# Optimization experiments

Hardware: AMD Instinct MI355X
Metric: run time of the kernel (lower is better)

The kernel has to match this reference:

```python
import jax, jax.numpy as jnp
import numpy as np

N_NODES = 50000
N_EDGES = 800000
N_POS = 200000
N_NEG = 200000
D_IN = 128
D_OUT = 128
NEG_SLOPE = 0.2  # DGL GATConv default leaky_relu slope


def setup_inputs() -> dict:
    key = jax.random.key(0)
    ks = jax.random.split(key, 12)
    inp = {
        "x": jax.random.normal(ks[0], (N_NODES, D_IN), dtype=jnp.float32),
        "W": jax.random.normal(ks[1], (D_IN, D_OUT), dtype=jnp.float32) / np.sqrt(D_IN),
        "attn_l": jax.random.normal(ks[2], (D_OUT,), dtype=jnp.float32) / np.sqrt(D_OUT),
        "attn_r": jax.random.normal(ks[3], (D_OUT,), dtype=jnp.float32) / np.sqrt(D_OUT),
        "bias": jnp.zeros((D_OUT,), dtype=jnp.float32),
        "src": jax.random.randint(ks[4], (N_EDGES,), 0, N_NODES, dtype=jnp.int32),
        "dst": jax.random.randint(ks[5], (N_EDGES,), 0, N_NODES, dtype=jnp.int32),
        "pos_src": jax.random.randint(ks[6], (N_POS,), 0, N_NODES, dtype=jnp.int32),
        "pos_dst": jax.random.randint(ks[7], (N_POS,), 0, N_NODES, dtype=jnp.int32),
        "neg_src": jax.random.randint(ks[8], (N_NEG,), 0, N_NODES, dtype=jnp.int32),
        "neg_dst": jax.random.randint(ks[9], (N_NEG,), 0, N_NODES, dtype=jnp.int32),
    }
    return inp


def _gat_conv(x, W, attn_l, attn_r, bias, src, dst):
    # DGL GATConv, num_heads=1, feat_drop=0, activation=relu
    feat = x @ W                               # [N, D_OUT]
    el = feat @ attn_l                         # [N]
    er = feat @ attn_r                         # [N]
    e = jax.nn.leaky_relu(el[src] + er[dst], NEG_SLOPE)  # [E]
    # edge softmax grouped by destination node
    m = jax.ops.segment_max(e, dst, num_segments=N_NODES)   # [N]
    ee = jnp.exp(e - m[dst])
    s = jax.ops.segment_sum(ee, dst, num_segments=N_NODES)  # [N]
    a = ee / s[dst]                            # [E]
    # weighted message aggregation
    h = jax.ops.segment_sum(a[:, None] * feat[src], dst, num_segments=N_NODES)
    return jax.nn.relu(h + bias)               # [N, D_OUT]


def reference(x, W, attn_l, attn_r, bias, src, dst, pos_src, pos_dst, neg_src, neg_dst):
    h = _gat_conv(x, W, attn_l, attn_r, bias, src, dst)
    # ScorePredictor: u_dot_v on each scoring graph -> [E, 1]
    pos_score = jnp.sum(h[pos_src] * h[pos_dst], axis=-1, keepdims=True)
    neg_score = jnp.sum(h[neg_src] * h[neg_dst], axis=-1, keepdims=True)
    return (pos_score, neg_score)
```

## Files before the change

kernel.cpp:

```cpp
#include <hip/hip_runtime.h>
#include <hip/hip_bf16.h>
#include <cstdint>
#include <cstddef>

#define N_NODES 50000
#define N_EDGES 800000
#define N_POS   200000
#define N_NEG   200000
#define DIM     128
#define NEG_SLOPE 0.2f

#define BUCK_SHIFT 5
#define BUCK_NODES 32
#define NBUCK 1563
#define SLABCAP 768
#define BIN_CHUNK 2048
#define NB_BIN 391
#define N_EDGE4 200000

typedef _Float16 half8 __attribute__((ext_vector_type(8)));
typedef float    floatx4 __attribute__((ext_vector_type(4)));

__global__ __launch_bounds__(256) void gemm_feat(
    const float* __restrict__ x, const float* __restrict__ W,
    const float* __restrict__ attn_l, const float* __restrict__ attn_r,
    half8* __restrict__ feat16, float* __restrict__ el, float* __restrict__ er,
    int n)
{
  __shared__ _Float16 xt[64 * 128];
  __shared__ _Float16 wt[128 * 128];
  const int tid = threadIdx.x;
  const int row0 = blockIdx.x * 64;
  const int lane = tid & 63;
  const int wv = tid >> 6;
  const int ql = lane & 15;
  const int quad = lane >> 4;

  {
    const int k = tid >> 1;
    const int n0 = (tid & 1) * 64;
#pragma unroll 4
    for (int j = 0; j < 64; j += 4) {
      const float4 v = *(const float4*)&W[(size_t)k * DIM + n0 + j];
      const float vv[4] = {v.x, v.y, v.z, v.w};
#pragma unroll
      for (int u = 0; u < 4; ++u) {
        const int nn = n0 + j + u;
        wt[nn * 128 + ((((k >> 3) ^ (nn & 15)) << 3) | (k & 7))] = (_Float16)vv[u];
      }
    }
  }
  {
    const int r = tid >> 2;
    const int grow = row0 + r;
    const int c0 = (tid & 3) * 32;
#pragma unroll
    for (int cc = 0; cc < 32; cc += 8) {
      const int c = c0 + cc;
      float4 v0 = make_float4(0.f, 0.f, 0.f, 0.f);
      float4 v1 = make_float4(0.f, 0.f, 0.f, 0.f);
      if (grow < n) {
        const float* sp = &x[(size_t)grow * DIM + c];
        v0 = *(const float4*)(sp);
        v1 = *(const float4*)(sp + 4);
      }
      half8 h;
      h[0] = (_Float16)v0.x; h[1] = (_Float16)v0.y;
      h[2] = (_Float16)v0.z; h[3] = (_Float16)v0.w;
      h[4] = (_Float16)v1.x; h[5] = (_Float16)v1.y;
      h[6] = (_Float16)v1.z; h[7] = (_Float16)v1.w;
      const int chunk = c >> 3;
      *(half8*)&xt[r * 128 + ((chunk ^ (r & 15)) << 3)] = h;
    }
  }
  __syncthreads();

  floatx4 acc[8];
#pragma unroll
  for (int t = 0; t < 8; ++t) acc[t] = (floatx4){0.f, 0.f, 0.f, 0.f};

  const int arow = wv * 16 + ql;
  half8 af[4];
#pragma unroll
  for (int s = 0; s < 4; ++s) {
    const int chunk = s * 4 + quad;
    af[s] = *(half8*)&xt[arow * 128 + ((chunk ^ ql) << 3)];
  }
#pragma unroll
  for (int t = 0; t < 8; ++t) {
    const int brow = t * 16 + ql;
#pragma unroll
    for (int s = 0; s < 4; ++s) {
      const int chunk = s * 4 + quad;
      const half8 bf = *(half8*)&wt[brow * 128 + ((chunk ^ ql) << 3)];
      acc[t] = __builtin_amdgcn_mfma_f32_16x16x32_f16(af[s], bf, acc[t], 0, 0, 0);
    }
  }

  {
    float al8[8], ar8[8];
#pragma unroll
    for (int t = 0; t < 8; ++t) {
      al8[t] = attn_l[t * 16 + ql];
      ar8[t] = attn_r[t * 16 + ql];
    }
    float pl[4] = {0.f, 0.f, 0.f, 0.f};
    float pr[4] = {0.f, 0.f, 0.f, 0.f};
#pragma unroll
    for (int t = 0; t < 8; ++t)
#pragma unroll
      for (int r = 0; r < 4; ++r) {
        pl[r] = fmaf(acc[t][r], al8[t], pl[r]);
        pr[r] = fmaf(acc[t][r], ar8[t], pr[r]);
      }
#pragma unroll
    for (int o = 1; o < 16; o <<= 1)
#pragma unroll
      for (int r = 0; r < 4; ++r) {
        pl[r] += __shfl_xor(pl[r], o, 64);
        pr[r] += __shfl_xor(pr[r], o, 64);
      }
    if (ql == 0) {
#pragma unroll
      for (int r = 0; r < 4; ++r) {
        const int grow = row0 + wv * 16 + quad * 4 + r;
        if (grow < n) { el[grow] = pl[r]; er[grow] = pr[r]; }
      }
    }
  }

#pragma unroll
  for (int t = 0; t < 8; ++t)
#pragma unroll
    for (int r = 0; r < 4; ++r)
      xt[(wv * 16 + quad * 4 + r) * 128 + t * 16 + ql] = (_Float16)acc[t][r];
  __syncthreads();
  {
    const int r = tid >> 2;
    const int grow = row0 + r;
    if (grow < n) {
      const int c0 = (tid & 3) * 32;
#pragma unroll
      for (int cc = 0; cc < 32; cc += 8) {
        const half8 h = *(half8*)&xt[r * 128 + c0 + cc];
        feat16[(size_t)grow * 16 + ((c0 + cc) >> 3)] = h;
      }
    }
  }
}

__global__ __launch_bounds__(256) void bin_kernel(
    const int4* __restrict__ src4, const int4* __restrict__ dst4,
    unsigned int* __restrict__ slab, int* __restrict__ slab_cursor)
{
  __shared__ int hist[NBUCK];
  __shared__ int base_s[NBUCK];
  __shared__ int cur[NBUCK];
  const int tid = threadIdx.x;
  const int i4base = blockIdx.x * 512;
  const int i40 = i4base + tid;
  const int i41 = i4base + 256 + tid;
  const bool v0 = i40 < N_EDGE4;
  const bool v1 = i41 < N_EDGE4;

  for (int i = tid; i < NBUCK; i += 256) { hist[i] = 0; cur[i] = 0; }
  int4 d0 = v0 ? dst4[i40] : make_int4(0, 0, 0, 0);
  int4 d1 = v1 ? dst4[i41] : make_int4(0, 0, 0, 0);
  __syncthreads();

  if (v0) {
    atomicAdd(&hist[d0.x >> BUCK_SHIFT], 1);
    atomicAdd(&hist[d0.y >> BUCK_SHIFT], 1);
    atomicAdd(&hist[d0.z >> BUCK_SHIFT], 1);
    atomicAdd(&hist[d0.w >> BUCK_SHIFT], 1);
  }
  if (v1) {
    atomicAdd(&hist[d1.x >> BUCK_SHIFT], 1);
    atomicAdd(&hist[d1.y >> BUCK_SHIFT], 1);
    atomicAdd(&hist[d1.z >> BUCK_SHIFT], 1);
    atomicAdd(&hist[d1.w >> BUCK_SHIFT], 1);
  }
  int4 s0 = v0 ? src4[i40] : make_int4(0, 0, 0, 0);
  int4 s1 = v1 ? src4[i41] : make_int4(0, 0, 0, 0);
  __syncthreads();

  for (int i = tid; i < NBUCK; i += 256) {
    const int h = hist[i];
    base_s[i] = h ? atomicAdd(&slab_cursor[i], h) : 0;
  }
  __syncthreads();

  int dd[8] = {d0.x, d0.y, d0.z, d0.w, d1.x, d1.y, d1.z, d1.w};
  int ss[8] = {s0.x, s0.y, s0.z, s0.w, s1.x, s1.y, s1.z, s1.w};
#pragma unroll
  for (int u = 0; u < 8; ++u) {
    if (u < 4 ? v0 : v1) {
      const int d = dd[u];
      const int bk = d >> BUCK_SHIFT;
      const int p = atomicAdd(&cur[bk], 1);
      int idx = base_s[bk] + p;
      if (idx >= SLABCAP) idx = SLABCAP - 1;
      slab[(size_t)bk * SLABCAP + idx] =
          ((unsigned int)ss[u] << BUCK_SHIFT) | (unsigned int)(d & (BUCK_NODES - 1));
    }
  }
}

__global__ __launch_bounds__(256) void aggregate_kernel(
    const half8* __restrict__ feat16, const float* __restrict__ el,
    const float* __restrict__ er,
    const unsigned int* __restrict__ slab, const int* __restrict__ slab_cursor,
    const float* __restrict__ bias, half8* __restrict__ h16)
{
  __shared__ unsigned int csr[SLABCAP];
  __shared__ int cnt_l[BUCK_NODES];
  __shared__ int start_l[BUCK_NODES];
  __shared__ int cur_l[BUCK_NODES];
  const int b = blockIdx.x;
  const int tid = threadIdx.x;
  const int cnt = min(slab_cursor[b], SLABCAP);
  const unsigned int* sb = slab + (size_t)b * SLABCAP;
  const int node0 = b << BUCK_SHIFT;

  if (tid < BUCK_NODES) cnt_l[tid] = 0;
  __syncthreads();
  for (int i = tid; i < cnt; i += 256)
    atomicAdd(&cnt_l[sb[i] & (BUCK_NODES - 1)], 1);
  __syncthreads();
  if (tid < 64) {
    const int v = (tid < BUCK_NODES) ? cnt_l[tid] : 0;
    int inc = v;
#pragma unroll
    for (int d = 1; d < 32; d <<= 1) {
      const int t = __shfl_up(inc, d, 64);
      if (tid >= d) inc += t;
    }
    if (tid < BUCK_NODES) { start_l[tid] = inc - v; cur_l[tid] = 0; }
  }
  __syncthreads();
  for (int i = tid; i < cnt; i += 256) {
    const unsigned int r = sb[i];
    const int p = atomicAdd(&cur_l[r & (BUCK_NODES - 1)], 1);
    csr[start_l[r & (BUCK_NODES - 1)] + p] = r;
  }
  __syncthreads();

  const int lane = tid & 63;
  const int ql = lane & 15;
  const int qb = lane & 48;
  const int qid = (tid >> 6) * 4 + (lane >> 4);
  const float4 b0 = *(const float4*)&bias[ql * 8];
  const float4 b1 = *(const float4*)&bias[ql * 8 + 4];
  const float bb[8] = {b0.x, b0.y, b0.z, b0.w, b1.x, b1.y, b1.z, b1.w};

  for (int nl = qid; nl < BUCK_NODES; nl += 16) {
    const int node = node0 + nl;
    if (node >= N_NODES) break;
    const int beg = start_l[nl];
    const int c = cnt_l[nl];
    const float ern = er[node];

    float sp = 0.f;
    float acc[8];
#pragma unroll
    for (int k = 0; k < 8; ++k) acc[k] = 0.f;

    for (int t0 = 0; t0 < c; t0 += 16) {
      const int t = t0 + ql;
      const unsigned int r = csr[beg + ((t < c) ? t : (c - 1))];
      const int sid = (int)(r >> BUCK_SHIFT);
      float w = 0.f;
      if (t < c) {
        const float v = el[sid] + ern;
        const float e = (v > 0.f) ? v : NEG_SLOPE * v;
        w = __expf(e);
      }
      sp += w;
      const int nb = min(16, c - t0);
      int j = 0;
      for (; j + 4 <= nb; j += 4) {
        float wv[4]; int sv[4]; half8 fv[4];
#pragma unroll
        for (int u = 0; u < 4; ++u) {
          wv[u] = __shfl(w, qb + j + u, 64);
          sv[u] = __shfl(sid, qb + j + u, 64);
        }
#pragma unroll
        for (int u = 0; u < 4; ++u) fv[u] = feat16[(size_t)sv[u] * 16 + ql];
#pragma unroll
        for (int u = 0; u < 4; ++u)
#pragma unroll
          for (int k = 0; k < 8; ++k)
            acc[k] = fmaf(wv[u], (float)fv[u][k], acc[k]);
      }
      for (; j < nb; ++j) {
        const float wj = __shfl(w, qb + j, 64);
        const int sj = __shfl(sid, qb + j, 64);
        const half8 f = feat16[(size_t)sj * 16 + ql];
#pragma unroll
        for (int k = 0; k < 8; ++k) acc[k] = fmaf(wj, (float)f[k], acc[k]);
      }
    }

#pragma unroll
    for (int o = 1; o < 16; o <<= 1) sp += __shfl_xor(sp, o, 64);

    const float inv = (c > 0) ? 1.f / sp : 0.f;
    half8 o;
#pragma unroll
    for (int k = 0; k < 8; ++k)
      o[k] = (_Float16)fmaxf(acc[k] * inv + bb[k], 0.f);
    h16[(size_t)node * 16 + ql] = o;
  }
}

__global__ __launch_bounds__(256) void score_kernel(
    const half8* __restrict__ h16,
    const int* __restrict__ pos_src, const int* __restrict__ pos_dst,
    const int* __restrict__ neg_src, const int* __restrict__ neg_dst,
    float* __restrict__ out, int ntot)
{
  const int wid = (int)((blockIdx.x * blockDim.x + threadIdx.x) >> 6);
  const int lane = threadIdx.x & 63;
  const int q = lane >> 4;
  const int ql = lane & 15;
  const int base = (wid * 4 + q) * 4;

  int av[4], bv[4];
#pragma unroll
  for (int u = 0; u < 4; ++u) {
    const int p = base + u;
    int a = 0, b = 0;
    if (p < N_POS)      { a = pos_src[p]; b = pos_dst[p]; }
    else if (p < ntot)  { a = neg_src[p - N_POS]; b = neg_dst[p - N_POS]; }
    av[u] = a; bv[u] = b;
  }
  half8 ha[4], hb[4];
#pragma unroll
  for (int u = 0; u < 4; ++u) {
    ha[u] = h16[(size_t)av[u] * 16 + ql];
    hb[u] = h16[(size_t)bv[u] * 16 + ql];
  }
  float sum[4];
#pragma unroll
  for (int u = 0; u < 4; ++u) {
    float s = 0.f;
#pragma unroll
    for (int k = 0; k < 8; ++k) s = fmaf((float)ha[u][k], (float)hb[u][k], s);
#pragma unroll
    for (int o = 8; o > 0; o >>= 1) s += __shfl_xor(s, o, 64);
    sum[u] = s;
  }
  if (ql == 0) {
#pragma unroll
    for (int u = 0; u < 4; ++u) {
      const int p = base + u;
      if (p < ntot) out[p] = sum[u];
    }
  }
}

extern "C" void kernel_launch(void* const* d_in, const int* in_sizes, int n_in,
                              void* d_out, int out_size, void* d_ws, size_t ws_size,
                              hipStream_t stream) {
  const float* x      = (const float*)d_in[0];
  const float* W      = (const float*)d_in[1];
  const float* attn_l = (const float*)d_in[2];
  const float* attn_r = (const float*)d_in[3];
  const float* bias   = (const float*)d_in[4];
  const int* src      = (const int*)d_in[5];
  const int* dst      = (const int*)d_in[6];
  const int* pos_src  = (const int*)d_in[7];
  const int* pos_dst  = (const int*)d_in[8];
  const int* neg_src  = (const int*)d_in[9];
  const int* neg_dst  = (const int*)d_in[10];
  float* out = (float*)d_out;

  char* ws = (char*)d_ws;
  const size_t F16B = (size_t)N_NODES * DIM * sizeof(_Float16);
  half8* feat16          = (half8*)(ws);
  half8* h16             = (half8*)(ws + F16B);
  float* el              = (float*)(ws + 2 * F16B);
  float* er              = (float*)(ws + 2 * F16B + 200000);
  int*   slab_cursor     = (int*)  (ws + 2 * F16B + 400000);
  unsigned int* slab     = (unsigned int*)(ws + 2 * F16B + 406656);

  hipMemsetAsync(slab_cursor, 0, NBUCK * sizeof(int), stream);

  gemm_feat<<<(N_NODES + 63) / 64, 256, 0, stream>>>(
      x, W, attn_l, attn_r, feat16, el, er, N_NODES);
  bin_kernel<<<NB_BIN, 256, 0, stream>>>(
      (const int4*)src, (const int4*)dst, slab, slab_cursor);
  aggregate_kernel<<<NBUCK, 256, 0, stream>>>(
      feat16, el, er, slab, slab_cursor, bias, h16);
  score_kernel<<<((N_POS + N_NEG + 15) / 16 + 3) / 4, 256, 0, stream>>>(
      h16, pos_src, pos_dst, neg_src, neg_dst, out, N_POS + N_NEG);
}
```

Baseline: 190.1 us.

## Fuse edge binning into GEMM launch and pretranspose W once in prep kernel

Moves the edge-binning work and the feature GEMM into one launch with disjoint block ranges, so binning blocks run alongside GEMM blocks instead of in a separate serialized kernel. A small prep kernel converts W to fp16 in swizzled layout once and also zeroes the slab cursors, replacing the hipMemsetAsync. Each GEMM block now copies the prepared W tile from global memory instead of converting it itself. The cost is an extra tiny launch and a shared-memory union sized for the larger of the two roles, which may lower occupancy for the binning blocks.

```diff
diff --git a/kernel.cpp b/kernel.cpp
--- a/kernel.cpp
+++ b/kernel.cpp
@@ -14,41 +14,111 @@
 #define BUCK_NODES 32
 #define NBUCK 1563
 #define SLABCAP 768
-#define BIN_CHUNK 2048
 #define NB_BIN 391
 #define N_EDGE4 200000
+#define NB_GEMM 782
 
 typedef _Float16 half8 __attribute__((ext_vector_type(8)));
 typedef float    floatx4 __attribute__((ext_vector_type(4)));
 
-__global__ __launch_bounds__(256) void gemm_feat(
-    const float* __restrict__ x, const float* __restrict__ W,
+__global__ __launch_bounds__(256) void prep_kernel(
+    const float* __restrict__ W, _Float16* __restrict__ wt_g,
+    int* __restrict__ slab_cursor)
+{
+  const int tid = threadIdx.x;
+  for (int i = blockIdx.x * 256 + tid; i < NBUCK; i += 4 * 256)
+    slab_cursor[i] = 0;
+  const int k = blockIdx.x * 32 + (tid >> 3);
+  const int n0 = (tid & 7) * 16;
+#pragma unroll
+  for (int j = 0; j < 16; j += 4) {
+    const float4 v = *(const float4*)&W[(size_t)k * DIM + n0 + j];
+    const float vv[4] = {v.x, v.y, v.z, v.w};
+#pragma unroll
+    for (int u = 0; u < 4; ++u) {
+      const int nn = n0 + j + u;
+      wt_g[nn * 128 + ((((k >> 3) ^ (nn & 15)) << 3) | (k & 7))] = (_Float16)vv[u];
+    }
+  }
+}
+
+__global__ __launch_bounds__(256) void fused_gemm_bin(
+    const float* __restrict__ x, const _Float16* __restrict__ wt_g,
     const float* __restrict__ attn_l, const float* __restrict__ attn_r,
+    const int4* __restrict__ src4, const int4* __restrict__ dst4,
     half8* __restrict__ feat16, float* __restrict__ el, float* __restrict__ er,
-    int n)
+    unsigned int* __restrict__ slab, int* __restrict__ slab_cursor, int n)
 {
-  __shared__ _Float16 xt[64 * 128];
-  __shared__ _Float16 wt[128 * 128];
+  __shared__ char smem[49152];
   const int tid = threadIdx.x;
-  const int row0 = blockIdx.x * 64;
+
+  if (blockIdx.x < NB_BIN) {
+    int* hist   = (int*)smem;
+    int* base_s = hist + NBUCK;
+    int* cur    = base_s + NBUCK;
+    const int i4base = blockIdx.x * 512;
+    const int i40 = i4base + tid;
+    const int i41 = i4base + 256 + tid;
+    const bool v0 = i40 < N_EDGE4;
+    const bool v1 = i41 < N_EDGE4;
+
+    for (int i = tid; i < NBUCK; i += 256) { hist[i] = 0; cur[i] = 0; }
+    int4 d0 = v0 ? dst4[i40] : make_int4(0, 0, 0, 0);
+    int4 d1 = v1 ? dst4[i41] : make_int4(0, 0, 0, 0);
+    __syncthreads();
+
+    if (v0) {
+      atomicAdd(&hist[d0.x >> BUCK_SHIFT], 1);
+      atomicAdd(&hist[d0.y >> BUCK_SHIFT], 1);
+      atomicAdd(&hist[d0.z >> BUCK_SHIFT], 1);
+      atomicAdd(&hist[d0.w >> BUCK_SHIFT], 1);
+    }
+    if (v1) {
+      atomicAdd(&hist[d1.x >> BUCK_SHIFT], 1);
+      atomicAdd(&hist[d1.y >> BUCK_SHIFT], 1);
+      atomicAdd(&hist[d1.z >> BUCK_SHIFT], 1);
+      atomicAdd(&hist[d1.w >> BUCK_SHIFT], 1);
+    }
+    int4 s0 = v0 ? src4[i40] : make_int4(0, 0, 0, 0);
+    int4 s1 = v1 ? src4[i41] : make_int4(0, 0, 0, 0);
+    __syncthreads();
+
+    for (int i = tid; i < NBUCK; i += 256) {
+      const int h = hist[i];
+      base_s[i] = h ? atomicAdd(&slab_cursor[i], h) : 0;
+    }
+    __syncthreads();
+
+    int dd[8] = {d0.x, d0.y, d0.z, d0.w, d1.x, d1.y, d1.z, d1.w};
+    int ss[8] = {s0.x, s0.y, s0.z, s0.w, s1.x, s1.y, s1.z, s1.w};
+#pragma unroll
+    for (int u = 0; u < 8; ++u) {
+      if (u < 4 ? v0 : v1) {
+        const int d = dd[u];
+        const int bk = d >> BUCK_SHIFT;
+        const int p = atomicAdd(&cur[bk], 1);
+        int idx = base_s[bk] + p;
+        if (idx >= SLABCAP) idx = SLABCAP - 1;
+        slab[(size_t)bk * SLABCAP + idx] =
+            ((unsigned int)ss[u] << BUCK_SHIFT) | (unsigned int)(d & (BUCK_NODES - 1));
+      }
+    }
+    return;
+  }
+
+  _Float16* xt = (_Float16*)smem;
+  _Float16* wt = (_Float16*)(smem + 16384);
+  const int row0 = (blockIdx.x - NB_BIN) * 64;
   const int lane = tid & 63;
   const int wv = tid >> 6;
   const int ql = lane & 15;
   const int quad = lane >> 4;
 
   {
-    const int k = tid >> 1;
-    const int n0 = (tid & 1) * 64;
-#pragma unroll 4
-    for (int j = 0; j < 64; j += 4) {
-      const float4 v = *(const float4*)&W[(size_t)k * DIM + n0 + j];
-      const float vv[4] = {v.x, v.y, v.z, v.w};
-#pragma unroll
-      for (int u = 0; u < 4; ++u) {
-        const int nn = n0 + j + u;
-        wt[nn * 128 + ((((k >> 3) ^ (nn & 15)) << 3) | (k & 7))] = (_Float16)vv[u];
-      }
-    }
+    const half8* s = (const half8*)wt_g;
+    half8* d = (half8*)wt;
+#pragma unroll
+    for (int i = 0; i < 8; ++i) d[tid + i * 256] = s[tid + i * 256];
   }
   {
     const int r = tid >> 2;
@@ -145,63 +215,6 @@
         const half8 h = *(half8*)&xt[r * 128 + c0 + cc];
         feat16[(size_t)grow * 16 + ((c0 + cc) >> 3)] = h;
       }
-    }
-  }
-}
-
-__global__ __launch_bounds__(256) void bin_kernel(
-    const int4* __restrict__ src4, const int4* __restrict__ dst4,
-    unsigned int* __restrict__ slab, int* __restrict__ slab_cursor)
-{
-  __shared__ int hist[NBUCK];
-  __shared__ int base_s[NBUCK];
-  __shared__ int cur[NBUCK];
-  const int tid = threadIdx.x;
-  const int i4base = blockIdx.x * 512;
-  const int i40 = i4base + tid;
-  const int i41 = i4base + 256 + tid;
-  const bool v0 = i40 < N_EDGE4;
-  const bool v1 = i41 < N_EDGE4;
-
-  for (int i = tid; i < NBUCK; i += 256) { hist[i] = 0; cur[i] = 0; }
-  int4 d0 = v0 ? dst4[i40] : make_int4(0, 0, 0, 0);
-  int4 d1 = v1 ? dst4[i41] : make_int4(0, 0, 0, 0);
-  __syncthreads();
-
-  if (v0) {
-    atomicAdd(&hist[d0.x >> BUCK_SHIFT], 1);
-    atomicAdd(&hist[d0.y >> BUCK_SHIFT], 1);
-    atomicAdd(&hist[d0.z >> BUCK_SHIFT], 1);
-    atomicAdd(&hist[d0.w >> BUCK_SHIFT], 1);
-  }
-  if (v1) {
-    atomicAdd(&hist[d1.x >> BUCK_SHIFT], 1);
-    atomicAdd(&hist[d1.y >> BUCK_SHIFT], 1);
-    atomicAdd(&hist[d1.z >> BUCK_SHIFT], 1);
-    atomicAdd(&hist[d1.w >> BUCK_SHIFT], 1);
-  }
-  int4 s0 = v0 ? src4[i40] : make_int4(0, 0, 0, 0);
-  int4 s1 = v1 ? src4[i41] : make_int4(0, 0, 0, 0);
-  __syncthreads();
-
-  for (int i = tid; i < NBUCK; i += 256) {
-    const int h = hist[i];
-    base_s[i] = h ? atomicAdd(&slab_cursor[i], h) : 0;
-  }
-  __syncthreads();
-
-  int dd[8] = {d0.x, d0.y, d0.z, d0.w, d1.x, d1.y, d1.z, d1.w};
-  int ss[8] = {s0.x, s0.y, s0.z, s0.w, s1.x, s1.y, s1.z, s1.w};
-#pragma unroll
-  for (int u = 0; u < 8; ++u) {
-    if (u < 4 ? v0 : v1) {
-      const int d = dd[u];
-      const int bk = d >> BUCK_SHIFT;
-      const int p = atomicAdd(&cur[bk], 1);
-      int idx = base_s[bk] + p;
-      if (idx >= SLABCAP) idx = SLABCAP - 1;
-      slab[(size_t)bk * SLABCAP + idx] =
-          ((unsigned int)ss[u] << BUCK_SHIFT) | (unsigned int)(d & (BUCK_NODES - 1));
     }
   }
 }
@@ -378,19 +391,19 @@
 
   char* ws = (char*)d_ws;
   const size_t F16B = (size_t)N_NODES * DIM * sizeof(_Float16);
+  const size_t SLAB_B = (size_t)NBUCK * SLABCAP * sizeof(unsigned int);
   half8* feat16          = (half8*)(ws);
   half8* h16             = (half8*)(ws + F16B);
   float* el              = (float*)(ws + 2 * F16B);
   float* er              = (float*)(ws + 2 * F16B + 200000);
   int*   slab_cursor     = (int*)  (ws + 2 * F16B + 400000);
   unsigned int* slab     = (unsigned int*)(ws + 2 * F16B + 406656);
-
-  hipMemsetAsync(slab_cursor, 0, NBUCK * sizeof(int), stream);
-
-  gemm_feat<<<(N_NODES + 63) / 64, 256, 0, stream>>>(
-      x, W, attn_l, attn_r, feat16, el, er, N_NODES);
-  bin_kernel<<<NB_BIN, 256, 0, stream>>>(
-      (const int4*)src, (const int4*)dst, slab, slab_cursor);
+  _Float16* wt_g         = (_Float16*)(ws + 2 * F16B + 406656 + SLAB_B);
+
+  prep_kernel<<<4, 256, 0, stream>>>(W, wt_g, slab_cursor);
+  fused_gemm_bin<<<NB_BIN + NB_GEMM, 256, 0, stream>>>(
+      x, wt_g, attn_l, attn_r, (const int4*)src, (const int4*)dst,
+      feat16, el, er, slab, slab_cursor, N_NODES);
   aggregate_kernel<<<NBUCK, 256, 0, stream>>>(
       feat16, el, er, slab, slab_cursor, bias, h16);
   score_kernel<<<((N_POS + N_NEG + 15) / 16 + 3) / 4, 256, 0, stream>>>(
```

Measured after the change: 172.7 us. 9.1% less time.
